# Performance work log

Hardware: AMD Instinct MI355X
Metric: run time of the kernel (lower is better)

Reference implementation:

```python
import jax, jax.numpy as jnp
import numpy as np

D_MODEL = 1024
GEOM_DIM = 32
CLAMP_VALUE = 10.0


def setup_inputs() -> dict:
    key = jax.random.key(0)
    k1, k2, k3 = jax.random.split(key, 3)
    B, N = 4, 2048
    H = jax.random.normal(k1, (B, N, D_MODEL), dtype=jnp.float32)
    B_prev = jax.random.normal(k2, (B, N, N), dtype=jnp.float32)
    # geom_proj weight, init std=0.001 as in the torch module
    W = jax.random.normal(k3, (GEOM_DIM, D_MODEL), dtype=jnp.float32) * 0.001
    alpha = jnp.asarray(1.0, dtype=jnp.float32)
    beta = jnp.asarray(0.05, dtype=jnp.float32)
    return {"H": H, "B_prev": B_prev, "W": W, "alpha": alpha, "beta": beta}


def reference(H, B_prev, W, alpha, beta):
    # Low-rank projection: G [B, N, geom_dim]
    G = jnp.einsum("bnd,kd->bnk", H, W)
    G_sq = jnp.sum(G * G, axis=-1)  # [B, N]
    # Pairwise squared distance: [B, N, N]
    gram = jnp.einsum("bik,bjk->bij", G, G)
    dist = G_sq[:, :, None] + G_sq[:, None, :] - 2.0 * gram
    dist = jnp.maximum(dist, 0.0)
    # EMA bias update with clamp
    B_next = alpha * B_prev - beta * dist
    B_next = jnp.clip(B_next, -CLAMP_VALUE, CLAMP_VALUE)
    return B_next
```

## Files before the change

kernel.cpp:

```cpp
#include <hip/hip_runtime.h>


typedef __attribute__((ext_vector_type(8))) short short8;
typedef __attribute__((ext_vector_type(4))) short short4v;
typedef __attribute__((ext_vector_type(4))) float floatx4;

static __device__ __forceinline__ short bf16_bits(float f) {
    union { float f; unsigned int u; } v; v.f = f;
    unsigned int u = v.u;
    u += 0x7FFFu + ((u >> 16) & 1u);
    return (short)(u >> 16);
}

static __device__ __forceinline__ float bf16_to_f32(unsigned short h) {
    union { unsigned int u; float f; } v; v.u = ((unsigned int)h) << 16;
    return v.f;
}

__global__ __launch_bounds__(256) void k0_wcast(const float* __restrict__ W,
                                                short* __restrict__ Wb) {
    const int f = blockIdx.x * 256 + threadIdx.x;
    const float4 v = *(const float4*)(W + (long)f * 4);
    short4v s;
    s[0] = bf16_bits(v.x); s[1] = bf16_bits(v.y);
    s[2] = bf16_bits(v.z); s[3] = bf16_bits(v.w);
    *(short4v*)(Wb + (long)f * 4) = s;
}

__global__ __launch_bounds__(256) void k1_proj(const float* __restrict__ H,
                                               const short* __restrict__ Wb,
                                               unsigned short* __restrict__ G,
                                               float* __restrict__ Q) {
    const int blk  = blockIdx.x;
    const int t    = threadIdx.x;
    const int w    = t >> 6;
    const int lane = t & 63;
    const int m    = lane & 15;
    const int quad = lane >> 4;

    __shared__ short sH[16 * 1032];

    const float* Hb = H + (long)blk * 16384;
    #pragma unroll
    for (int it = 0; it < 8; ++it) {
        const int f  = t + it * 256;
        const int r  = f >> 7;
        const int c8 = f & 127;
        const float4 v0 = *(const float4*)(Hb + r * 1024 + c8 * 8);
        const float4 v1 = *(const float4*)(Hb + r * 1024 + c8 * 8 + 4);
        short8 sv;
        sv[0] = bf16_bits(v0.x); sv[1] = bf16_bits(v0.y);
        sv[2] = bf16_bits(v0.z); sv[3] = bf16_bits(v0.w);
        sv[4] = bf16_bits(v1.x); sv[5] = bf16_bits(v1.y);
        sv[6] = bf16_bits(v1.z); sv[7] = bf16_bits(v1.w);
        *(short8*)&sH[r * 1032 + c8 * 8] = sv;
    }
    __syncthreads();

    const int kq = w * 256 + quad * 8;
    const short* wb0 = Wb + (long)m * 1024 + kq;
    const short* wb1 = Wb + (long)(m + 16) * 1024 + kq;

    floatx4 acc0 = {0.f, 0.f, 0.f, 0.f};
    floatx4 acc1 = {0.f, 0.f, 0.f, 0.f};

    short8 b0 = *(const short8*)wb0;
    short8 b1 = *(const short8*)wb1;

    #pragma unroll
    for (int s = 0; s < 8; ++s) {
        short8 nb0, nb1;
        if (s < 7) {
            nb0 = *(const short8*)(wb0 + (s + 1) * 32);
            nb1 = *(const short8*)(wb1 + (s + 1) * 32);
        }
        const short8 af = *(const short8*)&sH[m * 1032 + kq + s * 32];
        acc0 = __builtin_amdgcn_mfma_f32_16x16x32_bf16(af, b0, acc0, 0, 0, 0);
        acc1 = __builtin_amdgcn_mfma_f32_16x16x32_bf16(af, b1, acc1, 0, 0, 0);
        if (s < 7) { b0 = nb0; b1 = nb1; }
    }

    __shared__ float red[4][16][32];
    #pragma unroll
    for (int r = 0; r < 4; ++r) {
        red[w][quad * 4 + r][m]      = acc0[r];
        red[w][quad * 4 + r][m + 16] = acc1[r];
    }
    __syncthreads();
    for (int e = t; e < 512; e += 256) {
        const int mm = e >> 5, nn = e & 31;
        float v = red[0][mm][nn] + red[1][mm][nn] + red[2][mm][nn] + red[3][mm][nn];
        const unsigned short hb = (unsigned short)bf16_bits(v);
        G[(long)(blk * 16 + mm) * 32 + nn] = hb;
        red[0][mm][nn] = bf16_to_f32(hb);
    }
    __syncthreads();
    if (t < 16) {
        float s = 0.f;
        #pragma unroll
        for (int nn = 0; nn < 32; ++nn) { const float v = red[0][t][nn]; s += v * v; }
        Q[blk * 16 + t] = s;
    }
}

__global__ __launch_bounds__(256, 8) void k2_update(const float* __restrict__ Bp,
                                                    const unsigned short* __restrict__ G,
                                                    const float* __restrict__ Q,
                                                    const float* __restrict__ alphap,
                                                    const float* __restrict__ betap,
                                                    float* __restrict__ out) {
    const int b  = blockIdx.z;
    const int i0 = blockIdx.y * 64;
    const int jc = blockIdx.x;
    const int t  = threadIdx.x;
    const int w    = t >> 6;
    const int lane = t & 63;
    const int m    = lane & 15;
    const int quad = lane >> 4;

    const int i = i0 + w * 16 + m;
    const long rowoff = ((long)b * 2048 + i) * 2048 + jc * 128;

    const short* Gg = (const short*)G;
    const short8 bfi = *(const short8*)&Gg[((long)(b * 2048 + i)) * 32 + quad * 8];
    const float qi    = Q[b * 2048 + i];
    const float alpha = alphap[0];
    const float beta  = betap[0];

    const float* bpp    = Bp + rowoff + quad * 4;
    float*       op     = out + rowoff + quad * 4;
    const short* gjbase = Gg + ((long)(b * 2048 + jc * 128 + m)) * 32 + quad * 8;
    const float* qjbase = Q + (long)b * 2048 + jc * 128 + quad * 4;

    #pragma unroll
    for (int jt = 0; jt < 8; ++jt) {
        const short8  afj = *(const short8*)(gjbase + (long)jt * 16 * 32);
        const floatx4 qj  = *(const floatx4*)(qjbase + jt * 16);
        const floatx4 bv  = *(const floatx4*)(bpp + jt * 16);

        floatx4 z = {0.f, 0.f, 0.f, 0.f};
        const floatx4 acc = __builtin_amdgcn_mfma_f32_16x16x32_bf16(afj, bfi, z, 0, 0, 0);

        floatx4 ov;
        #pragma unroll
        for (int r = 0; r < 4; ++r) {
            float d = qi + qj[r] - 2.f * acc[r];
            d = fmaxf(d, 0.f);
            ov[r] = fminf(fmaxf(alpha * bv[r] - beta * d, -10.f), 10.f);
        }
        *(floatx4*)(op + jt * 16) = ov;
    }
}

extern "C" void kernel_launch(void* const* d_in, const int* in_sizes, int n_in,
                              void* d_out, int out_size, void* d_ws, size_t ws_size,
                              hipStream_t stream) {
    const float* H     = (const float*)d_in[0];
    const float* Bp    = (const float*)d_in[1];
    const float* W     = (const float*)d_in[2];
    const float* alpha = (const float*)d_in[3];
    const float* beta  = (const float*)d_in[4];
    float* out = (float*)d_out;

    unsigned short* G = (unsigned short*)d_ws;
    float* Q  = (float*)((char*)d_ws + 8192 * 32 * 2);
    short* Wb = (short*)((char*)d_ws + 8192 * 32 * 2 + 8192 * 4);

    k0_wcast<<<32, 256, 0, stream>>>(W, Wb);
    k1_proj<<<512, 256, 0, stream>>>(H, Wb, G, Q);

    dim3 g2(16, 32, 4);
    k2_update<<<g2, 256, 0, stream>>>(Bp, G, Q, alpha, beta, out);
}
```

Before: 162.6 us.

## Stream B_prev through LDS with async global_load_lds double buffering

Restructures the bias-update kernel so each block covers 512 columns in eight 64-column chunks. B_prev tiles are copied directly into LDS with global_load_lds and double-buffered, so the next chunk's load overlaps the MFMA distance computation for the current one. Distances go through LDS so that output stores become row-contiguous, fully coalesced float4 writes. In exchange it uses about 49KB of LDS per block, launches a quarter as many blocks, and adds explicit waitcnt and barrier synchronisation, which may reduce occupancy in a kernel that is purely bandwidth-bound.

```diff
diff --git a/kernel.cpp b/kernel.cpp
--- a/kernel.cpp
+++ b/kernel.cpp
@@ -103,53 +103,95 @@
     }
 }
 
-__global__ __launch_bounds__(256, 8) void k2_update(const float* __restrict__ Bp,
-                                                    const unsigned short* __restrict__ G,
-                                                    const float* __restrict__ Q,
-                                                    const float* __restrict__ alphap,
-                                                    const float* __restrict__ betap,
-                                                    float* __restrict__ out) {
+__global__ __launch_bounds__(256) void k2_update(const float* __restrict__ Bp,
+                                                 const unsigned short* __restrict__ G,
+                                                 const float* __restrict__ Q,
+                                                 const float* __restrict__ alphap,
+                                                 const float* __restrict__ betap,
+                                                 float* __restrict__ out) {
+    __shared__ float sBp[2][4096];
+    __shared__ float sDv[64 * 68];
+
     const int b  = blockIdx.z;
     const int i0 = blockIdx.y * 64;
-    const int jc = blockIdx.x;
+    const int J0 = blockIdx.x * 512;
     const int t  = threadIdx.x;
     const int w    = t >> 6;
     const int lane = t & 63;
     const int m    = lane & 15;
     const int quad = lane >> 4;
 
-    const int i = i0 + w * 16 + m;
-    const long rowoff = ((long)b * 2048 + i) * 2048 + jc * 128;
-
     const short* Gg = (const short*)G;
-    const short8 bfi = *(const short8*)&Gg[((long)(b * 2048 + i)) * 32 + quad * 8];
-    const float qi    = Q[b * 2048 + i];
+    const short8 bfi = *(const short8*)&Gg[((long)(b * 2048 + i0 + w * 16 + m)) * 32 + quad * 8];
+    const float qi    = Q[b * 2048 + i0 + w * 16 + m];
     const float alpha = alphap[0];
     const float beta  = betap[0];
 
-    const float* bpp    = Bp + rowoff + quad * 4;
-    float*       op     = out + rowoff + quad * 4;
-    const short* gjbase = Gg + ((long)(b * 2048 + jc * 128 + m)) * 32 + quad * 8;
-    const float* qjbase = Q + (long)b * 2048 + jc * 128 + quad * 4;
-
-    #pragma unroll
-    for (int jt = 0; jt < 8; ++jt) {
-        const short8  afj = *(const short8*)(gjbase + (long)jt * 16 * 32);
-        const floatx4 qj  = *(const floatx4*)(qjbase + jt * 16);
-        const floatx4 bv  = *(const floatx4*)(bpp + jt * 16);
-
-        floatx4 z = {0.f, 0.f, 0.f, 0.f};
-        const floatx4 acc = __builtin_amdgcn_mfma_f32_16x16x32_bf16(afj, bfi, z, 0, 0, 0);
-
-        floatx4 ov;
+    const float* dma_base = Bp + ((long)(b * 2048 + i0 + w * 16 + (lane >> 4))) * 2048
+                               + J0 + (lane & 15) * 4;
+
+#define GLOAD_LDS(gsrc, ldst) \
+    __builtin_amdgcn_global_load_lds((const __attribute__((address_space(1))) void*)(gsrc), \
+                                     (__attribute__((address_space(3))) void*)(ldst), 16, 0, 0)
+
+    #pragma unroll
+    for (int n = 0; n < 4; ++n)
+        GLOAD_LDS(dma_base + n * 4 * 2048, &sBp[0][w * 1024 + n * 256]);
+    __builtin_amdgcn_sched_barrier(0);
+
+    for (int c = 0; c < 8; ++c) {
+        const int cur = c & 1;
+        const int jcg = J0 + c * 64;
+
         #pragma unroll
-        for (int r = 0; r < 4; ++r) {
-            float d = qi + qj[r] - 2.f * acc[r];
-            d = fmaxf(d, 0.f);
-            ov[r] = fminf(fmaxf(alpha * bv[r] - beta * d, -10.f), 10.f);
-        }
-        *(floatx4*)(op + jt * 16) = ov;
-    }
+        for (int jt = 0; jt < 4; ++jt) {
+            const short8 afj = *(const short8*)&Gg[((long)(b * 2048 + jcg + jt * 16 + m)) * 32 + quad * 8];
+            const floatx4 qj = *(const floatx4*)&Q[b * 2048 + jcg + jt * 16 + quad * 4];
+            floatx4 z = {0.f, 0.f, 0.f, 0.f};
+            const floatx4 acc = __builtin_amdgcn_mfma_f32_16x16x32_bf16(afj, bfi, z, 0, 0, 0);
+            floatx4 dv;
+            #pragma unroll
+            for (int r = 0; r < 4; ++r)
+                dv[r] = beta * fmaxf(qi + qj[r] - 2.f * acc[r], 0.f);
+            *(floatx4*)&sDv[(w * 16 + m) * 68 + jt * 16 + quad * 4] = dv;
+        }
+
+        __builtin_amdgcn_sched_barrier(0);
+        if (c < 7) {
+            #pragma unroll
+            for (int n = 0; n < 4; ++n)
+                GLOAD_LDS(dma_base + n * 4 * 2048 + (c + 1) * 64,
+                          &sBp[cur ^ 1][w * 1024 + n * 256]);
+        }
+        __builtin_amdgcn_sched_barrier(0);
+
+        if (c < 7) { asm volatile("s_waitcnt vmcnt(4)" ::: "memory"); }
+        else       { asm volatile("s_waitcnt vmcnt(0)" ::: "memory"); }
+        __builtin_amdgcn_sched_barrier(0);
+        asm volatile("s_waitcnt lgkmcnt(0)" ::: "memory");
+        __builtin_amdgcn_sched_barrier(0);
+        __builtin_amdgcn_s_barrier();
+        __builtin_amdgcn_sched_barrier(0);
+
+        #pragma unroll
+        for (int k = 0; k < 4; ++k) {
+            const int row = (t >> 4) + k * 16;
+            const float4 bv = *(const float4*)&sBp[cur][t * 4 + k * 1024];
+            const float4 dv = *(const float4*)&sDv[row * 68 + (t & 15) * 4];
+            float4 ov;
+            ov.x = fminf(fmaxf(alpha * bv.x - dv.x, -10.f), 10.f);
+            ov.y = fminf(fmaxf(alpha * bv.y - dv.y, -10.f), 10.f);
+            ov.z = fminf(fmaxf(alpha * bv.z - dv.z, -10.f), 10.f);
+            ov.w = fminf(fmaxf(alpha * bv.w - dv.w, -10.f), 10.f);
+            *(float4*)(out + ((long)(b * 2048 + i0 + row)) * 2048 + jcg + (t & 15) * 4) = ov;
+        }
+
+        asm volatile("s_waitcnt lgkmcnt(0)" ::: "memory");
+        __builtin_amdgcn_sched_barrier(0);
+        __builtin_amdgcn_s_barrier();
+        __builtin_amdgcn_sched_barrier(0);
+    }
+#undef GLOAD_LDS
 }
 
 extern "C" void kernel_launch(void* const* d_in, const int* in_sizes, int n_in,
@@ -169,6 +211,6 @@
     k0_wcast<<<32, 256, 0, stream>>>(W, Wb);
     k1_proj<<<512, 256, 0, stream>>>(H, Wb, G, Q);
 
-    dim3 g2(16, 32, 4);
+    dim3 g2(4, 32, 4);
     k2_update<<<g2, 256, 0, stream>>>(Bp, G, Q, alpha, beta, out);
 }
```

Measured after the change: 161.0 us. No clear change (-1.0%).
